# Kernel optimization log

Measured on AMD Instinct MI355X. Metric: run time of the kernel, lower is better.

Reference implementation:

```python
import jax, jax.numpy as jnp
import numpy as np

EMBED_DIM = 768
NUM_HEADS = 12
KEY_DIM = EMBED_DIM // NUM_HEADS
B, S = 2, 2048

def _xavier(key, shape):
    # xavier_uniform over last-two dims (fan_in = shape[-2], fan_out = shape[-1])
    fan_in, fan_out = shape[-2], shape[-1]
    limit = jnp.sqrt(6.0 / (fan_in + fan_out)).astype(jnp.float32)
    return jax.random.uniform(key, shape, jnp.float32, -limit, limit)

def setup_inputs() -> dict:
    key = jax.random.key(0)
    kq, kk, kv, kwq, kwk, kwv, kw, km = jax.random.split(key, 8)
    q = jax.random.normal(kq, (B, S, EMBED_DIM), jnp.float32)
    k = jax.random.normal(kk, (B, S, EMBED_DIM), jnp.float32)
    v = jax.random.normal(kv, (B, S, EMBED_DIM), jnp.float32)
    # per-head projection weights stacked: [H, E, Dk]
    Wq = _xavier(kwq, (NUM_HEADS, EMBED_DIM, KEY_DIM))
    Wk = _xavier(kwk, (NUM_HEADS, EMBED_DIM, KEY_DIM))
    Wv = _xavier(kwv, (NUM_HEADS, EMBED_DIM, KEY_DIM))
    W = _xavier(kw, (EMBED_DIM, EMBED_DIM))
    mask = jax.random.randint(km, (B, 1, S, S), 0, 2).astype(jnp.int32)
    return {"q": q, "k": k, "v": v, "mask": mask, "Wq": Wq, "Wk": Wk, "Wv": Wv, "W": W}

def reference(q, k, v, mask, Wq, Wk, Wv, W):
    scale = 1.0 / jnp.sqrt(jnp.asarray(KEY_DIM, q.dtype))
    Q = jnp.einsum('bse,hed->bhsd', q, Wq)  # [B,H,S,Dk]
    K = jnp.einsum('bse,hed->bhsd', k, Wk)
    V = jnp.einsum('bse,hed->bhsd', v, Wv)
    Z = jnp.einsum('bhsd,bhtd->bhst', Q, K) * scale  # [B,H,S,S]
    Z = jnp.where(mask == 0, jnp.asarray(-1e9, Z.dtype), Z)
    score = jax.nn.softmax(Z, axis=-1)
    out = jnp.einsum('bhst,bhtd->bhsd', score, V)  # [B,H,S,Dk]
    # concat heads along last dim (head order = list order)
    concat = out.transpose(0, 2, 1, 3).reshape(q.shape[0], q.shape[1], EMBED_DIM)
    return concat @ W
```

## Files before the change

kernel.cpp:

```cpp
#include <hip/hip_runtime.h>
#include <stdint.h>

typedef uint16_t u16;
typedef __attribute__((ext_vector_type(8))) short bf16x8;
typedef __attribute__((ext_vector_type(4))) float f32x4;
typedef __attribute__((ext_vector_type(16))) float f32x16;

#define EMB 768
#define NH 12
#define DK 64
#define BB 2
#define SS 2048
#define SCL 0.1803368801111244f
#define M0  24.0f

__device__ __forceinline__ u16 f2bf(float x) {
  union { float f; uint32_t u; } v; v.f = x;
  uint32_t r = v.u + 0x7fffu + ((v.u >> 16) & 1u);
  return (u16)(r >> 16);
}

__device__ __forceinline__ uint32_t pk2(float a, float b) {
  uint32_t d;
  asm("v_cvt_pk_bf16_f32 %0, %1, %2" : "=v"(d) : "v"(a), "v"(b));
  return d;
}

__device__ __forceinline__ void gld16(const u16* g, u16* l) {
  __builtin_amdgcn_global_load_lds((const __attribute__((address_space(1))) void*)g,
                                   (__attribute__((address_space(3))) void*)l, 16, 0, 0);
}

__global__ void pack_all(const float* __restrict__ wq, const float* __restrict__ wk,
                         const float* __restrict__ wv, const float* __restrict__ w,
                         const int* __restrict__ mask,
                         u16* __restrict__ wqkvT, u16* __restrict__ wT,
                         uint64_t* __restrict__ bits) {
  uint32_t tl = blockIdx.x * 256 + threadIdx.x;
  const uint32_t WTOT = 4u * EMB * EMB;
  if (tl < WTOT) {
    int z = tl / (EMB * EMB);
    int t = tl - z * (EMB * EMB);
    int n = t / EMB, e = t - n * EMB;
    if (z < 3) {
      const float* src = z == 0 ? wq : (z == 1 ? wk : wv);
      float vv = src[((n >> 6) * EMB + e) * DK + (n & 63)];
      if (z == 0) vv *= SCL;
      wqkvT[(size_t)z * EMB * EMB + t] = f2bf(vv);
    } else {
      wT[t] = f2bf(w[e * EMB + n]);
    }
  } else {
    uint32_t widx = tl - WTOT;
    uint32_t wv64 = widx >> 6;
    uint32_t lane = widx & 63;
    uint32_t b  = wv64 >> 12;
    uint32_t qg = (wv64 >> 6) & 63;
    uint32_t tg = wv64 & 63;
    uint32_t c = lane & 31, hi = lane >> 5;
    const int* mp = mask + (((size_t)b * 2048 + qg * 32 + c) * 2048 + tg * 32 + hi * 4);
    int4 q0 = *(const int4*)mp;
    int4 q1 = *(const int4*)(mp + 8);
    int4 q2 = *(const int4*)(mp + 16);
    int4 q3 = *(const int4*)(mp + 24);
    uint64_t* wout = bits + (size_t)wv64 * 16;
    unsigned long long ball;
#define BAL(u, arr)                                                   \
    ball = __ballot(arr.x != 0); if (lane == 0) wout[u * 4 + 0] = ball; \
    ball = __ballot(arr.y != 0); if (lane == 0) wout[u * 4 + 1] = ball; \
    ball = __ballot(arr.z != 0); if (lane == 0) wout[u * 4 + 2] = ball; \
    ball = __ballot(arr.w != 0); if (lane == 0) wout[u * 4 + 3] = ball;
    BAL(0, q0) BAL(1, q1) BAL(2, q2) BAL(3, q3)
#undef BAL
  }
}

#define GEMM_MFMA_BODY64(Ab, Bb)                                                \
    bf16x8 af[2], bfr[4];                                                       \
    _Pragma("unroll")                                                           \
    for (int i = 0; i < 2; ++i)                                                 \
      af[i] = *(const bf16x8*)((Ab) + (wr * 32 + i * 16 + c) * 32 + qx * 8);    \
    _Pragma("unroll")                                                           \
    for (int j = 0; j < 4; ++j)                                                 \
      bfr[j] = *(const bf16x8*)((Bb) + (wc * 64 + j * 16 + c) * 32 + qx * 8);   \
    _Pragma("unroll")                                                           \
    for (int i = 0; i < 2; ++i)                                                 \
      _Pragma("unroll")                                                         \
      for (int j = 0; j < 4; ++j)                                               \
        acc[i][j] = __builtin_amdgcn_mfma_f32_16x16x32_bf16(af[i], bfr[j], acc[i][j], 0, 0, 0);

__device__ __forceinline__ void gemm_f32A_pipe(const float* __restrict__ A,
                                               const u16* __restrict__ Bt,
                                               int m0, int n0, u16* As, u16* Bs,
                                               f32x4 (&acc)[2][4]) {
  const int tid = threadIdx.x;
  const int lane = tid & 63, quad = lane >> 4, c = lane & 15;
  const int wr = (tid >> 6) >> 1, wc = (tid >> 6) & 1;
  const int qx = quad ^ ((c >> 1) & 3);
  const int arow = tid >> 2, aslot = tid & 3;
  const int awslot = aslot ^ ((arow >> 1) & 3);
  float4 a0, a1;
#define LOAD_A(kk)                                                     \
  {                                                                    \
    const float* src = A + (size_t)(m0 + arow) * EMB + (kk) + aslot * 8; \
    a0 = *(const float4*)src; a1 = *(const float4*)(src + 4);          \
  }
#define ISSUE_B(kk, buf)                                               \
  _Pragma("unroll")                                                    \
  for (int r = 0; r < 2; ++r) {                                        \
    int bo = r * 4096 + tid * 16;    \
    int brow = bo >> 6, bslot = (bo >> 4) & 3;                         \
    gld16(Bt + (size_t)(n0 + brow) * EMB + (kk) + (bslot ^ ((brow >> 1) & 3)) * 8, \
          Bs + (buf) * 4096 + (bo >> 1));         \
  }
  LOAD_A(0); ISSUE_B(0, 0);
  for (int kk = 0; kk < EMB; kk += 32) {
    const int buf = (kk >> 5) & 1;
    {
      uint4 pkv = { pk2(a0.x, a0.y), pk2(a0.z, a0.w),
                    pk2(a1.x, a1.y), pk2(a1.z, a1.w) };
      *(uint4*)(As + buf * 2048 + arow * 32 + awslot * 8) = pkv;
    }
    __syncthreads();
    if (kk + 32 < EMB) { LOAD_A(kk + 32); ISSUE_B(kk + 32, buf ^ 1); }
    const u16* Ab = As + buf * 2048;
    const u16* Bb = Bs + buf * 4096;
    GEMM_MFMA_BODY64(Ab, Bb)
  }
#undef LOAD_A
#undef ISSUE_B
}

__device__ __forceinline__ void gemm_bf16A_pipe(const u16* __restrict__ A,
                                                const u16* __restrict__ Bt,
                                                int m0, int n0, u16* As, u16* Bs,
                                                f32x4 (&acc)[2][4]) {
  const int tid = threadIdx.x;
  const int lane = tid & 63, quad = lane >> 4, c = lane & 15;
  const int wr = (tid >> 6) >> 1, wc = (tid >> 6) & 1;
  const int qx = quad ^ ((c >> 1) & 3);
#define ISSUE_AB(kk, buf)                                              \
  {                                                                    \
    int arow_ = tid >> 2, aslot_ = tid & 3;                            \
    gld16(A + (size_t)(m0 + arow_) * EMB + (kk) + (aslot_ ^ ((arow_ >> 1) & 3)) * 8, \
          As + (buf) * 2048 + tid * 8);                                \
    _Pragma("unroll")                                                  \
    for (int r = 0; r < 2; ++r) {                                      \
      int bo = r * 4096 + tid * 16;                                    \
      int brow = bo >> 6, bslot = (bo >> 4) & 3;                       \
      gld16(Bt + (size_t)(n0 + brow) * EMB + (kk) + (bslot ^ ((brow >> 1) & 3)) * 8, \
            Bs + (buf) * 4096 + (bo >> 1));                            \
    }                                                                  \
  }
  ISSUE_AB(0, 0);
  for (int kk = 0; kk < EMB; kk += 32) {
    const int buf = (kk >> 5) & 1;
    __syncthreads();
    if (kk + 32 < EMB) { ISSUE_AB(kk + 32, buf ^ 1); }
    const u16* Ab = As + buf * 2048;
    const u16* Bb = Bs + buf * 4096;
    GEMM_MFMA_BODY64(Ab, Bb)
  }
#undef ISSUE_AB
}

__launch_bounds__(256, 4)
__global__ void gemm_qkv(const float* __restrict__ q, const float* __restrict__ k,
                         const float* __restrict__ v, const u16* __restrict__ wt3,
                         u16* __restrict__ Qp, u16* __restrict__ Kp, u16* __restrict__ Vt) {
  __shared__ __align__(16) u16 As[2 * 64 * 32];
  __shared__ __align__(16) u16 Bs[2 * 128 * 32];
  const int id = blockIdx.x;
  const int xcd = id & 7, s = id >> 3;
  const int panel = xcd * 24 + s / 6;
  const int ntile = s - (s / 6) * 6;
  const int z = panel >> 6, mt = panel & 63;
  const int m0 = mt * 64, n0 = ntile * 128;
  const float* A = z == 0 ? q : (z == 1 ? k : v);
  const u16* Bt = wt3 + (size_t)z * EMB * EMB;
  f32x4 acc[2][4];
  const f32x4 fz = {0.f, 0.f, 0.f, 0.f};
#pragma unroll
  for (int i = 0; i < 2; ++i)
#pragma unroll
    for (int j = 0; j < 4; ++j) acc[i][j] = fz;
  gemm_f32A_pipe(A, Bt, m0, n0, As, Bs, acc);
  const int tid = threadIdx.x, lane = tid & 63, quad = lane >> 4, c = lane & 15;
  const int wr = (tid >> 6) >> 1, wc = (tid >> 6) & 1;
  if (z < 2) {
    u16* C = z == 0 ? Qp : Kp;
#pragma unroll
    for (int i = 0; i < 2; ++i)
#pragma unroll
      for (int j = 0; j < 4; ++j) {
        int row = m0 + wr * 32 + i * 16 + quad * 4;
        int col = n0 + wc * 64 + j * 16 + c;
#pragma unroll
        for (int r = 0; r < 4; r += 2) {
          uint32_t d = pk2(acc[i][j][r], acc[i][j][r + 1]);
          C[(size_t)(row + r) * EMB + col] = (u16)d;
          C[(size_t)(row + r + 1) * EMB + col] = (u16)(d >> 16);
        }
      }
  } else {
#pragma unroll
    for (int i = 0; i < 2; ++i)
#pragma unroll
      for (int j = 0; j < 4; ++j) {
        int row = m0 + wr * 32 + i * 16 + quad * 4;
        int col = n0 + wc * 64 + j * 16 + c;
        int b = row >> 11, ss = row & 2047;
        int h = col >> 6, d = col & 63;
        uint2 pk = { pk2(acc[i][j][0], acc[i][j][1]), pk2(acc[i][j][2], acc[i][j][3]) };
        *(uint2*)(Vt + ((size_t)(b * NH + h) * DK + d) * SS + ss) = pk;
      }
  }
}

__launch_bounds__(256, 4)
__global__ void gemm_out(const u16* __restrict__ A, const u16* __restrict__ Bt,
                         float* __restrict__ C) {
  __shared__ __align__(16) u16 As[2 * 64 * 32];
  __shared__ __align__(16) u16 Bs[2 * 128 * 32];
  const int id = blockIdx.x;
  const int xcd = id & 7, s = id >> 3;
  const int panel = xcd * 8 + s / 6;
  const int ntile = s - (s / 6) * 6;
  const int m0 = panel * 64, n0 = ntile * 128;
  f32x4 acc[2][4];
  const f32x4 fz = {0.f, 0.f, 0.f, 0.f};
#pragma unroll
  for (int i = 0; i < 2; ++i)
#pragma unroll
    for (int j = 0; j < 4; ++j) acc[i][j] = fz;
  gemm_bf16A_pipe(A, Bt, m0, n0, As, Bs, acc);
  const int tid = threadIdx.x, lane = tid & 63, quad = lane >> 4, c = lane & 15;
  const int wr = (tid >> 6) >> 1, wc = (tid >> 6) & 1;
#pragma unroll
  for (int i = 0; i < 2; ++i)
#pragma unroll
    for (int j = 0; j < 4; ++j)
#pragma unroll
      for (int r = 0; r < 4; ++r) {
        int row = m0 + wr * 32 + i * 16 + quad * 4 + r;
        int col = n0 + wc * 64 + j * 16 + c;
        C[(size_t)row * EMB + col] = acc[i][j][r];
      }
}

__launch_bounds__(512, 4)
__global__ void attn(const u16* __restrict__ Qp, const u16* __restrict__ Kp,
                     const u16* __restrict__ Vt, const uint64_t* __restrict__ MW,
                     u16* __restrict__ AO) {
  __shared__ __align__(16) u16 sm[2 * 128 * 72 + 2 * 64 * 136];
  u16* Ks0 = sm;
  u16* Vs0 = sm + 2 * 128 * 72;

  const int tid = threadIdx.x, lane = tid & 63;
  const int c = lane & 31, hi = lane >> 5;
  const int w = tid >> 6;
  const int wq2 = w >> 2, th = w & 3;

  const int wid = blockIdx.x;
  const int xcd = wid & 7, slot = wid >> 3;
  const int bh = xcd + 8 * (slot >> 5);
  const int mtile = slot & 31;
  const int b = bh / NH, h = bh - b * NH;
  const int m0 = mtile * 64;

  const size_t qkbase = (size_t)b * SS * EMB + (size_t)h * DK;
  const size_t vtbase = (size_t)bh * DK * SS;

  bf16x8 aq[4];
  {
    const u16* qr = Qp + qkbase + (size_t)(m0 + wq2 * 32 + c) * EMB + hi * 8;
    aq[0] = *(const bf16x8*)(qr);
    aq[1] = *(const bf16x8*)(qr + 16);
    aq[2] = *(const bf16x8*)(qr + 32);
    aq[3] = *(const bf16x8*)(qr + 48);
  }

  const int srK = tid >> 2, scK = (tid & 3) * 16;
  const int srV = tid >> 3, scV = (tid & 7) * 16;
  const u16* gK = Kp + qkbase + (size_t)srK * EMB + scK;
  const u16* gV = Vt + vtbase + (size_t)srV * SS + scV;
  bf16x8 kr0, kr1, vr0, vr1;
#define LOADKV(t0) {                                             \
    const u16* gk_ = gK + (size_t)(t0) * EMB;                    \
    kr0 = *(const bf16x8*)gk_; kr1 = *(const bf16x8*)(gk_ + 8);  \
    const u16* gv_ = gV + (t0);                                  \
    vr0 = *(const bf16x8*)gv_; vr1 = *(const bf16x8*)(gv_ + 8); }
#define STOREKV(buf) {                                           \
    u16* ks_ = Ks0 + (buf) * (128 * 72) + srK * 72 + scK;        \
    *(bf16x8*)ks_ = kr0; *(bf16x8*)(ks_ + 8) = kr1;              \
    u16* vs_ = Vs0 + (buf) * (64 * 136) + srV * 136 + scV;       \
    *(bf16x8*)vs_ = vr0; *(bf16x8*)(vs_ + 8) = vr1; }

  const int thu = __builtin_amdgcn_readfirstlane(th);
  const int qgu = __builtin_amdgcn_readfirstlane(mtile * 2 + wq2);
  const uint64_t* mwb = MW + (((size_t)b * 64 + qgu) * 64) * 16 + thu * 16;
#define LOADMSK(m, it) {                                         \
    const uint64_t* mp_ = mwb + (size_t)(it) * 64;               \
    _Pragma("unroll")                                            \
    for (int r_ = 0; r_ < 16; ++r_) m[r_] = mp_[r_]; }

  float fNEG = -1e9f, fM0 = -M0;
  float lr = 0.f;
  f32x16 o0, o1;
#pragma unroll
  for (int r_ = 0; r_ < 16; ++r_) { o0[r_] = 0.f; o1[r_] = 0.f; }

  uint64_t mA[16], mB[16];
  LOADKV(0); LOADMSK(mA, 0);

#define BODY(it, buf, mc, mn) {                                                   \
    STOREKV(buf);                                                                 \
    __syncthreads();                                                              \
    if ((it) < 15) { LOADKV(((it) + 1) * 128); LOADMSK(mn, (it) + 1); }           \
     \
    f32x16 s;                                                                     \
    _Pragma("unroll")                                                             \
    for (int r_ = 0; r_ < 16; ++r_) {                                             \
      float t_;                                                                   \
      asm("v_cndmask_b32 %0, %1, %2, %3"                                          \
          : "=v"(t_) : "v"(fNEG), "v"(fM0), "s"(mc[r_]));                         \
      s[r_] = t_;                                                                 \
    }                                                                             \
                                          \
    const u16* kb_ = Ks0 + (buf) * (128 * 72) + (th * 32 + c) * 72 + hi * 8;      \
    _Pragma("unroll")                                                             \
    for (int ks_ = 0; ks_ < 4; ++ks_) {                                           \
      bf16x8 kf_ = *(const bf16x8*)(kb_ + ks_ * 16);                              \
      s = __builtin_amdgcn_mfma_f32_32x32x16_bf16(kf_, aq[ks_], s, 0, 0, 0);      \
    }                                                                             \
                               \
    _Pragma("unroll")                                                             \
    for (int r_ = 0; r_ < 16; ++r_) s[r_] = __builtin_amdgcn_exp2f(s[r_]);        \
    lr += ((s[0] + s[1]) + (s[2] + s[3])) + ((s[4] + s[5]) + (s[6] + s[7]))       \
        + ((s[8] + s[9]) + (s[10] + s[11])) + ((s[12] + s[13]) + (s[14] + s[15]));\
                      \
    uint32_t x0 = pk2(s[0], s[1]),  x1 = pk2(s[2], s[3]);                         \
    uint32_t y0 = pk2(s[4], s[5]),  y1 = pk2(s[6], s[7]);                         \
    uint32_t z0 = pk2(s[8], s[9]),  z1 = pk2(s[10], s[11]);                       \
    uint32_t w0 = pk2(s[12], s[13]), w1 = pk2(s[14], s[15]);                      \
    asm("v_permlane32_swap_b32 %0, %1" : "+v"(x0), "+v"(y0));                     \
    asm("v_permlane32_swap_b32 %0, %1" : "+v"(x1), "+v"(y1));                     \
    asm("v_permlane32_swap_b32 %0, %1" : "+v"(z0), "+v"(w0));                     \
    asm("v_permlane32_swap_b32 %0, %1" : "+v"(z1), "+v"(w1));                     \
    bf16x8 pa0, pa1;                                                              \
    { union { uint32_t u[4]; bf16x8 v; } cv;                                      \
      cv.u[0] = x0; cv.u[1] = x1; cv.u[2] = y0; cv.u[3] = y1; pa0 = cv.v;         \
      cv.u[0] = z0; cv.u[1] = z1; cv.u[2] = w0; cv.u[3] = w1; pa1 = cv.v; }       \
                                  \
    const u16* vb_ = Vs0 + (buf) * (64 * 136) + c * 136 + th * 32 + hi * 8;       \
    {                                                                             \
      bf16x8 vf_;                                                                 \
      vf_ = *(const bf16x8*)(vb_);                                                \
      o0 = __builtin_amdgcn_mfma_f32_32x32x16_bf16(vf_, pa0, o0, 0, 0, 0);        \
      vf_ = *(const bf16x8*)(vb_ + 16);                                           \
      o0 = __builtin_amdgcn_mfma_f32_32x32x16_bf16(vf_, pa1, o0, 0, 0, 0);        \
      vf_ = *(const bf16x8*)(vb_ + 32 * 136);                                     \
      o1 = __builtin_amdgcn_mfma_f32_32x32x16_bf16(vf_, pa0, o1, 0, 0, 0);        \
      vf_ = *(const bf16x8*)(vb_ + 32 * 136 + 16);                                \
      o1 = __builtin_amdgcn_mfma_f32_32x32x16_bf16(vf_, pa1, o1, 0, 0, 0);        \
    } }

  for (int i2 = 0; i2 < 8; ++i2) {
    BODY(i2 * 2,     0, mA, mB)
    BODY(i2 * 2 + 1, 1, mB, mA)
  }
#undef BODY
#undef LOADKV
#undef STOREKV
#undef LOADMSK

  lr += __shfl_xor(lr, 32);
  __syncthreads();
  float* Of = (float*)sm;
  float* Lf = (float*)sm + 4 * 64 * 65;
  {
    int row = wq2 * 32 + c;
#pragma unroll
    for (int r_ = 0; r_ < 16; ++r_) {
      int d = (r_ & 3) + 8 * (r_ >> 2) + 4 * hi;
      Of[(th * 64 + row) * 65 + d]      = o0[r_];
      Of[(th * 64 + row) * 65 + 32 + d] = o1[r_];
    }
    if (hi == 0) Lf[row * 4 + th] = lr;
  }
  __syncthreads();
  {
    int qrow = tid >> 3, d0 = (tid & 7) * 8;
    float lt = Lf[qrow * 4 + 0] + Lf[qrow * 4 + 1] + Lf[qrow * 4 + 2] + Lf[qrow * 4 + 3];
    float inv = 1.f / fmaxf(lt, 1e-20f);
    float acc[8];
#pragma unroll
    for (int e = 0; e < 8; ++e) acc[e] = 0.f;
#pragma unroll
    for (int t_ = 0; t_ < 4; ++t_)
#pragma unroll
      for (int e = 0; e < 8; ++e) acc[e] += Of[(t_ * 64 + qrow) * 65 + d0 + e];
    uint32_t dw[4];
#pragma unroll
    for (int e = 0; e < 4; ++e) dw[e] = pk2(acc[2 * e] * inv, acc[2 * e + 1] * inv);
    *(uint4*)(AO + qkbase + (size_t)(m0 + qrow) * EMB + d0) = *(uint4*)dw;
  }
}

extern "C" void kernel_launch(void* const* d_in, const int* in_sizes, int n_in,
                              void* d_out, int out_size, void* d_ws, size_t ws_size,
                              hipStream_t stream) {
  const float* q  = (const float*)d_in[0];
  const float* k  = (const float*)d_in[1];
  const float* v  = (const float*)d_in[2];
  const int* mask = (const int*)d_in[3];
  const float* Wq = (const float*)d_in[4];
  const float* Wk = (const float*)d_in[5];
  const float* Wv = (const float*)d_in[6];
  const float* W  = (const float*)d_in[7];
  float* out = (float*)d_out;

  u16* Kp = (u16*)d_out;
  u16* Vt = (u16*)d_out + 3145728;

  u16* ws    = (u16*)d_ws;
  u16* Qp    = ws;
  u16* WqkvT = ws + 3145728;
  u16* WT    = ws + 3145728 + 1769472;
  uint64_t* mb64 = (uint64_t*)(ws + 5505024);
  u16* AO = Qp;

  pack_all<<<dim3(11264), 256, 0, stream>>>(Wq, Wk, Wv, W, mask, WqkvT, WT, mb64);
  gemm_qkv<<<dim3(1152), 256, 0, stream>>>(q, k, v, WqkvT, Qp, Kp, Vt);
  attn<<<dim3(768), 512, 0, stream>>>(Qp, Kp, Vt, mb64, AO);
  gemm_out<<<dim3(384), 256, 0, stream>>>(AO, WT, out);
}
```

Before: 224.6 us.

## Tile weight packing via LDS transpose and shrink output GEMM tiles

Result: faster. 217.0 us (-3.3%).

```diff
diff --git a/kernel.cpp b/kernel.cpp
--- a/kernel.cpp
+++ b/kernel.cpp
@@ -14,12 +14,6 @@
 #define SCL 0.1803368801111244f
 #define M0  24.0f
 
-__device__ __forceinline__ u16 f2bf(float x) {
-  union { float f; uint32_t u; } v; v.f = x;
-  uint32_t r = v.u + 0x7fffu + ((v.u >> 16) & 1u);
-  return (u16)(r >> 16);
-}
-
 __device__ __forceinline__ uint32_t pk2(float a, float b) {
   uint32_t d;
   asm("v_cvt_pk_bf16_f32 %0, %1, %2" : "=v"(d) : "v"(a), "v"(b));
@@ -36,22 +30,51 @@
                          const int* __restrict__ mask,
                          u16* __restrict__ wqkvT, u16* __restrict__ wT,
                          uint64_t* __restrict__ bits) {
-  uint32_t tl = blockIdx.x * 256 + threadIdx.x;
-  const uint32_t WTOT = 4u * EMB * EMB;
-  if (tl < WTOT) {
-    int z = tl / (EMB * EMB);
-    int t = tl - z * (EMB * EMB);
-    int n = t / EMB, e = t - n * EMB;
-    if (z < 3) {
+  __shared__ float L[65 * 64];
+  const int bid = blockIdx.x, tid = threadIdx.x;
+  if (bid < 576) {
+    const float* srcBase;
+    int srcRowStride;
+    u16* outBase;
+    float scale = 1.0f;
+    if (bid < 432) {
+      int z = bid / 144, rest = bid - z * 144;
+      int h = rest / 12, et = rest - h * 12;
       const float* src = z == 0 ? wq : (z == 1 ? wk : wv);
-      float vv = src[((n >> 6) * EMB + e) * DK + (n & 63)];
-      if (z == 0) vv *= SCL;
-      wqkvT[(size_t)z * EMB * EMB + t] = f2bf(vv);
+      srcBase = src + (size_t)h * (EMB * DK) + (size_t)(et * 64) * DK;
+      srcRowStride = DK;
+      outBase = wqkvT + (size_t)z * (EMB * EMB) + (size_t)(h * 64) * EMB + et * 64;
+      if (z == 0) scale = SCL;
     } else {
-      wT[t] = f2bf(w[e * EMB + n]);
+      int idx = bid - 432;
+      int nt = idx / 12, et = idx - nt * 12;
+      srcBase = w + (size_t)(et * 64) * EMB + nt * 64;
+      srcRowStride = EMB;
+      outBase = wT + (size_t)(nt * 64) * EMB + et * 64;
+    }
+    {
+      int e = tid >> 2, d0 = (tid & 3) * 16;
+      const float* s_ = srcBase + (size_t)e * srcRowStride + d0;
+      float4 v0 = *(const float4*)s_,       v1 = *(const float4*)(s_ + 4);
+      float4 v2 = *(const float4*)(s_ + 8), v3 = *(const float4*)(s_ + 12);
+      float tv[16] = { v0.x, v0.y, v0.z, v0.w, v1.x, v1.y, v1.z, v1.w,
+                       v2.x, v2.y, v2.z, v2.w, v3.x, v3.y, v3.z, v3.w };
+#pragma unroll
+      for (int j = 0; j < 16; ++j) L[e + 65 * (d0 + j)] = tv[j];
+    }
+    __syncthreads();
+    {
+      int d = tid >> 2, e0 = (tid & 3) * 16;
+      uint32_t pk[8];
+#pragma unroll
+      for (int j = 0; j < 8; ++j)
+        pk[j] = pk2(L[e0 + 2 * j + 65 * d] * scale, L[e0 + 2 * j + 1 + 65 * d] * scale);
+      u16* o = outBase + (size_t)d * EMB + e0;
+      *(uint4*)o = *(uint4*)pk;
+      *(uint4*)(o + 8) = *(uint4*)(pk + 4);
     }
   } else {
-    uint32_t widx = tl - WTOT;
+    uint32_t widx = (uint32_t)(bid - 576) * 256 + tid;
     uint32_t wv64 = widx >> 6;
     uint32_t lane = widx & 63;
     uint32_t b  = wv64 >> 12;
@@ -131,10 +154,10 @@
 #undef ISSUE_B
 }
 
-__device__ __forceinline__ void gemm_bf16A_pipe(const u16* __restrict__ A,
-                                                const u16* __restrict__ Bt,
-                                                int m0, int n0, u16* As, u16* Bs,
-                                                f32x4 (&acc)[2][4]) {
+__device__ __forceinline__ void gemm_bf16A_pipe64(const u16* __restrict__ A,
+                                                  const u16* __restrict__ Bt,
+                                                  int m0, int n0, u16* As, u16* Bs,
+                                                  f32x4 (&acc)[2][2]) {
   const int tid = threadIdx.x;
   const int lane = tid & 63, quad = lane >> 4, c = lane & 15;
   const int wr = (tid >> 6) >> 1, wc = (tid >> 6) & 1;
@@ -144,13 +167,10 @@
     int arow_ = tid >> 2, aslot_ = tid & 3;                            \
     gld16(A + (size_t)(m0 + arow_) * EMB + (kk) + (aslot_ ^ ((arow_ >> 1) & 3)) * 8, \
           As + (buf) * 2048 + tid * 8);                                \
-    _Pragma("unroll")                                                  \
-    for (int r = 0; r < 2; ++r) {                                      \
-      int bo = r * 4096 + tid * 16;                                    \
-      int brow = bo >> 6, bslot = (bo >> 4) & 3;                       \
-      gld16(Bt + (size_t)(n0 + brow) * EMB + (kk) + (bslot ^ ((brow >> 1) & 3)) * 8, \
-            Bs + (buf) * 4096 + (bo >> 1));                            \
-    }                                                                  \
+    int bo = tid * 16;               \
+    int brow = bo >> 6, bslot = (bo >> 4) & 3;                         \
+    gld16(Bt + (size_t)(n0 + brow) * EMB + (kk) + (bslot ^ ((brow >> 1) & 3)) * 8, \
+          Bs + (buf) * 2048 + (bo >> 1));                              \
   }
   ISSUE_AB(0, 0);
   for (int kk = 0; kk < EMB; kk += 32) {
@@ -158,8 +178,19 @@
     __syncthreads();
     if (kk + 32 < EMB) { ISSUE_AB(kk + 32, buf ^ 1); }
     const u16* Ab = As + buf * 2048;
-    const u16* Bb = Bs + buf * 4096;
-    GEMM_MFMA_BODY64(Ab, Bb)
+    const u16* Bb = Bs + buf * 2048;
+    bf16x8 af[2], bfr[2];
+#pragma unroll
+    for (int i = 0; i < 2; ++i)
+      af[i] = *(const bf16x8*)(Ab + (wr * 32 + i * 16 + c) * 32 + qx * 8);
+#pragma unroll
+    for (int j = 0; j < 2; ++j)
+      bfr[j] = *(const bf16x8*)(Bb + (wc * 32 + j * 16 + c) * 32 + qx * 8);
+#pragma unroll
+    for (int i = 0; i < 2; ++i)
+#pragma unroll
+      for (int j = 0; j < 2; ++j)
+        acc[i][j] = __builtin_amdgcn_mfma_f32_16x16x32_bf16(af[i], bfr[j], acc[i][j], 0, 0, 0);
   }
 #undef ISSUE_AB
 }
@@ -221,29 +252,29 @@
 __global__ void gemm_out(const u16* __restrict__ A, const u16* __restrict__ Bt,
                          float* __restrict__ C) {
   __shared__ __align__(16) u16 As[2 * 64 * 32];
-  __shared__ __align__(16) u16 Bs[2 * 128 * 32];
+  __shared__ __align__(16) u16 Bs[2 * 64 * 32];
   const int id = blockIdx.x;
   const int xcd = id & 7, s = id >> 3;
-  const int panel = xcd * 8 + s / 6;
-  const int ntile = s - (s / 6) * 6;
-  const int m0 = panel * 64, n0 = ntile * 128;
-  f32x4 acc[2][4];
+  const int panel = xcd * 8 + s / 12;
+  const int ntile = s - (s / 12) * 12;
+  const int m0 = panel * 64, n0 = ntile * 64;
+  f32x4 acc[2][2];
   const f32x4 fz = {0.f, 0.f, 0.f, 0.f};
 #pragma unroll
   for (int i = 0; i < 2; ++i)
 #pragma unroll
-    for (int j = 0; j < 4; ++j) acc[i][j] = fz;
-  gemm_bf16A_pipe(A, Bt, m0, n0, As, Bs, acc);
+    for (int j = 0; j < 2; ++j) acc[i][j] = fz;
+  gemm_bf16A_pipe64(A, Bt, m0, n0, As, Bs, acc);
   const int tid = threadIdx.x, lane = tid & 63, quad = lane >> 4, c = lane & 15;
   const int wr = (tid >> 6) >> 1, wc = (tid >> 6) & 1;
 #pragma unroll
   for (int i = 0; i < 2; ++i)
 #pragma unroll
-    for (int j = 0; j < 4; ++j)
+    for (int j = 0; j < 2; ++j)
 #pragma unroll
       for (int r = 0; r < 4; ++r) {
         int row = m0 + wr * 32 + i * 16 + quad * 4 + r;
-        int col = n0 + wc * 64 + j * 16 + c;
+        int col = n0 + wc * 32 + j * 16 + c;
         C[(size_t)row * EMB + col] = acc[i][j][r];
       }
 }
@@ -430,8 +461,8 @@
   uint64_t* mb64 = (uint64_t*)(ws + 5505024);
   u16* AO = Qp;
 
-  pack_all<<<dim3(11264), 256, 0, stream>>>(Wq, Wk, Wv, W, mask, WqkvT, WT, mb64);
+  pack_all<<<dim3(2624), 256, 0, stream>>>(Wq, Wk, Wv, W, mask, WqkvT, WT, mb64);
   gemm_qkv<<<dim3(1152), 256, 0, stream>>>(q, k, v, WqkvT, Qp, Kp, Vt);
   attn<<<dim3(768), 512, 0, stream>>>(Qp, Kp, Vt, mb64, AO);
-  gemm_out<<<dim3(384), 256, 0, stream>>>(AO, WT, out);
-}
+  gemm_out<<<dim3(768), 256, 0, stream>>>(AO, WT, out);
+}
```
